# Performance work log

Hardware: AMD Instinct MI355X
Metric: run time of the kernel (lower is better)

Reference implementation:

```python
import jax, jax.numpy as jnp
import numpy as np
import math

B, S, D, H = 2, 2048, 1024, 16
DH = D // H

def setup_inputs() -> dict:
    key = jax.random.key(0)
    ks = jax.random.split(key, 16)
    g = lambda k, shp, s=1.0: jax.random.normal(k, shp, dtype=jnp.float32) * s
    w = 1.0 / math.sqrt(D)
    return {
        "x": g(ks[0], (B, S, D)),
        "pos_emb": g(ks[1], (S, D)),
        "Wq": g(ks[2], (D, D), w), "bq": g(ks[3], (D,), 0.02),
        "Wk": g(ks[4], (D, D), w), "bk": g(ks[5], (D,), 0.02),
        "Wv": g(ks[6], (D, D), w), "bv": g(ks[7], (D,), 0.02),
        "Wo": g(ks[8], (D, D), w), "bo": g(ks[9], (D,), 0.02),
        "Wkr": g(ks[10], (D, D), w), "bkr": g(ks[11], (D,), 0.02),
        "u": g(ks[12], (H, DH)),
        "v": g(ks[13], (H, DH)),
    }

def _relative_shift(t):
    # t: [b, h, s, L] -> pad one zero column at front, reinterpret as
    # [b, h, L+1, s], drop first row -> [b, h, L, s] (matches torch view_as trick)
    b, h, s, L = t.shape
    t = jnp.pad(t, ((0, 0), (0, 0), (0, 0), (1, 0)))
    t = t.reshape(b, h, L + 1, s)
    return t[:, :, 1:, :]

def reference(x, pos_emb, Wq, bq, Wk, bk, Wv, bv, Wo, bo, Wkr, bkr, u, v):
    b, s, d = x.shape
    scale = 1.0 / math.sqrt(DH)
    # projections (memory=None, so keys/values come from x itself)
    q = (x @ Wq + bq).reshape(b, s, H, DH).transpose(0, 2, 1, 3)   # [b,h,s,dh]
    k = (x @ Wk + bk).reshape(b, s, H, DH).transpose(0, 2, 1, 3)   # [b,h,s,dh]
    val = (x @ Wv + bv).reshape(b, s, H, DH).transpose(0, 2, 1, 3)  # [b,h,s,dh]
    k_r = (pos_emb @ Wkr + bkr).reshape(s, H, DH)                   # [L,h,dh]
    # four score terms
    AC = jnp.einsum('bhid,bhjd->bhij', q, k)                         # [b,h,s,L]
    BD = _relative_shift(jnp.einsum('bhid,jhd->bhij', q, k_r))       # [b,h,L,s] (s==L)
    EF = jnp.einsum('hd,bhjd->bhj', u, k)[:, :, None, :]             # [b,h,1,L]
    GH = _relative_shift(jnp.einsum('hd,jhd->hj', v, k_r)[None, :, None, :])  # [1,h,L,1]
    attn_score = (AC + BD + EF + GH) * scale
    attn_prob = jax.nn.softmax(attn_score, axis=-1)
    out = jnp.einsum('bhij,bhjd->bhid', attn_prob, val)              # [b,h,s,dh]
    out = out.transpose(0, 2, 1, 3).reshape(b, s, d)
    return out @ Wo + bo
```

## Files before the change

kernel.cpp:

```cpp
#include <hip/hip_runtime.h>
#include <hip/hip_bf16.h>

#define S_LEN 2048
#define D_MODEL 1024
#define NH 16
#define DHEAD 64
#define NB 2

typedef __attribute__((ext_vector_type(8))) short bf16x8;
typedef __attribute__((ext_vector_type(4))) float f32x4;

__device__ __forceinline__ float bf2f(unsigned short u) {
    return __uint_as_float(((unsigned)u) << 16);
}
__device__ __forceinline__ unsigned short f2bf(float f) {
    unsigned x = __float_as_uint(f);
    x += 0x7fffu + ((x >> 16) & 1u);
    return (unsigned short)(x >> 16);
}

__global__ __launch_bounds__(256)
void convert_bf16(const float* __restrict__ in, unsigned short* __restrict__ out, int n4) {
    int i = blockIdx.x * 256 + threadIdx.x;
    if (i >= n4) return;
    float4 v = reinterpret_cast<const float4*>(in)[i];
    ushort4 o;
    o.x = f2bf(v.x); o.y = f2bf(v.y); o.z = f2bf(v.z); o.w = f2bf(v.w);
    reinterpret_cast<ushort4*>(out)[i] = o;
}

__global__ __launch_bounds__(256)
void convert_transpose(const float* __restrict__ in, unsigned short* __restrict__ out) {
    __shared__ float t[32][33];
    int k0 = blockIdx.y * 32, n0 = blockIdx.x * 32;
    int tx = threadIdx.x & 31, ty = threadIdx.x >> 5;
    #pragma unroll
    for (int r = ty; r < 32; r += 8) t[r][tx] = in[(size_t)(k0 + r) * D_MODEL + n0 + tx];
    __syncthreads();
    #pragma unroll
    for (int r = ty; r < 32; r += 8) out[(size_t)(n0 + r) * D_MODEL + k0 + tx] = f2bf(t[tx][r]);
}

template<int MODE>
__global__ __launch_bounds__(256)
void gemm_mfma(const unsigned short* __restrict__ A,
               const unsigned short* __restrict__ Wt,
               const float* __restrict__ bias,
               void* __restrict__ C, int M) {
    const int K = D_MODEL;
    __shared__ short As[128][72];
    __shared__ short Bs[128][72];
    int tid = threadIdx.x;
    int m0 = blockIdx.y * 128, n0 = blockIdx.x * 128;
    int lane = tid & 63, w = tid >> 6;
    int wm = (w >> 1) * 64, wn = (w & 1) * 64;
    int ls = lane & 15, lg = lane >> 4;

    f32x4 acc[4][4];
    #pragma unroll
    for (int ms = 0; ms < 4; ++ms)
        #pragma unroll
        for (int ns = 0; ns < 4; ++ns)
            acc[ms][ns] = (f32x4){0.f, 0.f, 0.f, 0.f};

    for (int k0 = 0; k0 < K; k0 += 64) {
        #pragma unroll
        for (int it = 0; it < 4; ++it) {
            int id = tid + it * 256;
            int row = id >> 3, ch = (id & 7) * 8;
            *reinterpret_cast<bf16x8*>(&As[row][ch]) =
                *reinterpret_cast<const bf16x8*>(A + (size_t)(m0 + row) * K + k0 + ch);
            *reinterpret_cast<bf16x8*>(&Bs[row][ch]) =
                *reinterpret_cast<const bf16x8*>(Wt + (size_t)(n0 + row) * K + k0 + ch);
        }
        __syncthreads();
        #pragma unroll
        for (int kk = 0; kk < 64; kk += 32) {
            bf16x8 af[4], bf[4];
            #pragma unroll
            for (int s = 0; s < 4; ++s) {
                af[s] = *reinterpret_cast<const bf16x8*>(&As[wm + s * 16 + ls][kk + lg * 8]);
                bf[s] = *reinterpret_cast<const bf16x8*>(&Bs[wn + s * 16 + ls][kk + lg * 8]);
            }
            #pragma unroll
            for (int ms = 0; ms < 4; ++ms)
                #pragma unroll
                for (int ns = 0; ns < 4; ++ns)
                    acc[ms][ns] = __builtin_amdgcn_mfma_f32_16x16x32_bf16(af[ms], bf[ns], acc[ms][ns], 0, 0, 0);
        }
        __syncthreads();
    }

    #pragma unroll
    for (int ns = 0; ns < 4; ++ns) {
        int n = n0 + wn + ns * 16 + ls;
        float bv = bias[n];
        #pragma unroll
        for (int ms = 0; ms < 4; ++ms) {
            #pragma unroll
            for (int e = 0; e < 4; ++e) {
                int m = m0 + wm + ms * 16 + lg * 4 + e;
                float v = acc[ms][ns][e] + bv;
                if (MODE == 0) {
                    ((float*)C)[(size_t)m * D_MODEL + n] = v;
                } else if (MODE == 1) {
                    int b = m >> 11, s = m & 2047, hh = n >> 6, dd = n & 63;
                    ((unsigned short*)C)[(((size_t)(b * NH + hh)) * S_LEN + s) * DHEAD + dd] = f2bf(v);
                } else if (MODE == 2) {
                    int s = m, hh = n >> 6, dd = n & 63;
                    ((unsigned short*)C)[(((size_t)hh) * S_LEN + s) * DHEAD + dd] = f2bf(v);
                } else {
                    int b = m >> 11, s = m & 2047, hh = n >> 6, dd = n & 63;
                    ((unsigned short*)C)[(((size_t)(b * NH + hh)) * DHEAD + dd) * S_LEN + s] = f2bf(v);
                }
            }
        }
    }
}

__global__ __launch_bounds__(256)
void ef_gh_kernel(const float* __restrict__ uv,
                  const unsigned short* __restrict__ kmat,
                  float* __restrict__ out, int total) {
    int idx = blockIdx.x * 256 + threadIdx.x;
    if (idx >= total) return;
    int pos = idx & (S_LEN - 1);
    int grp = idx >> 11;
    int hh = grp & (NH - 1);
    const unsigned short* krow = kmat + ((size_t)grp * S_LEN + pos) * DHEAD;
    const float* urow = uv + hh * DHEAD;
    float s = 0.f;
    #pragma unroll
    for (int d4 = 0; d4 < DHEAD; d4 += 4) {
        ushort4 kk = *reinterpret_cast<const ushort4*>(krow + d4);
        float4 uu = *reinterpret_cast<const float4*>(urow + d4);
        s += bf2f(kk.x) * uu.x + bf2f(kk.y) * uu.y
           + bf2f(kk.z) * uu.z + bf2f(kk.w) * uu.w;
    }
    out[idx] = s;
}

__global__ __launch_bounds__(256, 3)
void flash_mfma(const unsigned short* __restrict__ qT,
                const unsigned short* __restrict__ kT,
                const unsigned short* __restrict__ vTt,
                const unsigned short* __restrict__ krT,
                const float* __restrict__ EF,
                const float* __restrict__ GH,
                unsigned short* __restrict__ attn) {
    __shared__ unsigned short Ks[64][72];
    __shared__ unsigned short Vt[64][72];
    __shared__ unsigned short KRXU[128][72];
    __shared__ unsigned short Dp[65][68];
    __shared__ unsigned short Qs64[72];
    __shared__ float ef_s[64];
    __shared__ float gh_s[64];

    unsigned short* Pb = &KRXU[0][0];

    int tid = threadIdx.x;
    int bid = blockIdx.x;
    int ib = bid & 31;
    int bh = bid >> 5;
    int h = bh & (NH - 1);
    int b = bh >> 4;
    int i0 = ib * 64;

    int lane = tid & 63;
    int w = tid >> 6;
    int ls = lane & 15, lg = lane >> 4;

    const unsigned short* qbase = qT + (size_t)bh * S_LEN * DHEAD;
    const unsigned short* kbase = kT + (size_t)bh * S_LEN * DHEAD;
    const unsigned short* vtbase = vTt + (size_t)bh * DHEAD * S_LEN;
    const unsigned short* krbase = krT + (size_t)h * S_LEN * DHEAD;
    const float* efrow = EF + (size_t)bh * S_LEN;
    const float* ghrow = GH + (size_t)h * S_LEN;

    if (tid < 64) gh_s[tid] = ghrow[i0 + tid];
    if (tid < 8) {
        bf16x8 val = (bf16x8){0, 0, 0, 0, 0, 0, 0, 0};
        if (i0 + 64 < S_LEN)
            val = *reinterpret_cast<const bf16x8*>(qbase + (size_t)(i0 + 64) * DHEAD + tid * 8);
        *reinterpret_cast<bf16x8*>(&Qs64[tid * 8]) = val;
    }

    bf16x8 aq[2];
    #pragma unroll
    for (int kki = 0; kki < 2; ++kki)
        aq[kki] = *reinterpret_cast<const bf16x8*>(qbase + (size_t)(i0 + 16 * w + ls) * DHEAD + kki * 32 + lg * 8);

    f32x4 acc_o[4];
    #pragma unroll
    for (int nt = 0; nt < 4; ++nt) acc_o[nt] = (f32x4){0.f, 0.f, 0.f, 0.f};
    float m_r[4], l_r[4];
    #pragma unroll
    for (int e = 0; e < 4; ++e) { m_r[e] = -1e30f; l_r[e] = 0.f; }

    int nt0 = 3 - w;

    for (int jt = 0; jt < S_LEN / 64; ++jt) {
        int j0 = jt * 64;
        int dj = j0 - i0;

        #pragma unroll
        for (int it = 0; it < 2; ++it) {
            int s2 = tid + it * 256;
            int r = s2 >> 3, c8 = (s2 & 7) * 8;
            *reinterpret_cast<bf16x8*>(&Ks[r][c8]) =
                *reinterpret_cast<const bf16x8*>(kbase + (size_t)(j0 + r) * DHEAD + c8);
            *reinterpret_cast<bf16x8*>(&Vt[r][c8]) =
                *reinterpret_cast<const bf16x8*>(vtbase + (size_t)r * S_LEN + j0 + c8);
        }
        #pragma unroll
        for (int it = 0; it < 4; ++it) {
            int s2 = tid + it * 256;
            int v = s2 >> 3, c8 = (s2 & 7) * 8;
            int t = v + dj - 64;
            int gk = (t <= 0) ? (S_LEN - 1 + t) : (t - 1);
            bf16x8 val = (bf16x8){0, 0, 0, 0, 0, 0, 0, 0};
            if (gk >= 0)
                val = *reinterpret_cast<const bf16x8*>(krbase + (size_t)gk * DHEAD + c8);
            *reinterpret_cast<bf16x8*>(&KRXU[v][c8]) = val;
        }
        if (tid < 64) ef_s[tid] = efrow[j0 + tid];
        __syncthreads();

        f32x4 acc_ac[4];
        f32x4 acc_bd[5];
        #pragma unroll
        for (int nt = 0; nt < 4; ++nt) acc_ac[nt] = (f32x4){0.f, 0.f, 0.f, 0.f};
        #pragma unroll
        for (int i = 0; i < 5; ++i) acc_bd[i] = (f32x4){0.f, 0.f, 0.f, 0.f};

        #pragma unroll
        for (int kki = 0; kki < 2; ++kki) {
            #pragma unroll
            for (int nt = 0; nt < 4; ++nt) {
                bf16x8 bk = *reinterpret_cast<const bf16x8*>(&Ks[nt * 16 + ls][kki * 32 + lg * 8]);
                acc_ac[nt] = __builtin_amdgcn_mfma_f32_16x16x32_bf16(aq[kki], bk, acc_ac[nt], 0, 0, 0);
            }
            #pragma unroll
            for (int i = 0; i < 5; ++i) {
                bf16x8 bx = *reinterpret_cast<const bf16x8*>(&KRXU[(nt0 + i) * 16 + ls][kki * 32 + lg * 8]);
                acc_bd[i] = __builtin_amdgcn_mfma_f32_16x16x32_bf16(aq[kki], bx, acc_bd[i], 0, 0, 0);
            }
        }
        #pragma unroll
        for (int i = 0; i < 5; ++i) {
            int v = (nt0 + i) * 16 + ls;
            #pragma unroll
            for (int e = 0; e < 4; ++e) {
                int r = 16 * w + lg * 4 + e;
                int c = v + r - 64;
                if ((unsigned)c < 64u) Dp[r][c] = f2bf(acc_bd[i][e]);
            }
        }
        if (w == 3) {
            float s = 0.f;
            #pragma unroll
            for (int k8 = 0; k8 < 8; ++k8) {
                bf16x8 q8 = *reinterpret_cast<const bf16x8*>(&Qs64[k8 * 8]);
                bf16x8 x8 = *reinterpret_cast<const bf16x8*>(&KRXU[lane][k8 * 8]);
                #pragma unroll
                for (int e = 0; e < 8; ++e)
                    s += bf2f((unsigned short)q8[e]) * bf2f((unsigned short)x8[e]);
            }
            Dp[64][lane] = f2bf(s);
        }
        __syncthreads();

        float pv[4][4];
        #pragma unroll
        for (int nt = 0; nt < 4; ++nt) {
            int jl = nt * 16 + ls;
            float efv = ef_s[jl];
            #pragma unroll
            for (int e = 0; e < 4; ++e) {
                int il = 16 * w + lg * 4 + e;
                int t = dj + jl - il;
                float bd = (t == 1) ? 0.f : (t <= 0 ? bf2f(Dp[il][jl]) : bf2f(Dp[il + 1][jl]));
                pv[nt][e] = (acc_ac[nt][e] + bd + efv + gh_s[il]) * 0.125f;
            }
        }
        float fr[4];
        #pragma unroll
        for (int e = 0; e < 4; ++e) {
            float tm = fmaxf(fmaxf(pv[0][e], pv[1][e]), fmaxf(pv[2][e], pv[3][e]));
            #pragma unroll
            for (int off = 8; off >= 1; off >>= 1) tm = fmaxf(tm, __shfl_xor(tm, off));
            float mnew = fmaxf(m_r[e], tm);
            float fe = __expf(m_r[e] - mnew);
            float rs = 0.f;
            #pragma unroll
            for (int nt = 0; nt < 4; ++nt) {
                pv[nt][e] = __expf(pv[nt][e] - mnew);
                rs += pv[nt][e];
            }
            #pragma unroll
            for (int off = 8; off >= 1; off >>= 1) rs += __shfl_xor(rs, off);
            l_r[e] = l_r[e] * fe + rs;
            m_r[e] = mnew;
            fr[e] = fe;
        }
        #pragma unroll
        for (int nt = 0; nt < 4; ++nt)
            #pragma unroll
            for (int e = 0; e < 4; ++e)
                Pb[(16 * w + lg * 4 + e) * 72 + nt * 16 + ls] = f2bf(pv[nt][e]);
        __syncthreads();

        #pragma unroll
        for (int nt = 0; nt < 4; ++nt)
            #pragma unroll
            for (int e = 0; e < 4; ++e)
                acc_o[nt][e] *= fr[e];
        #pragma unroll
        for (int kki = 0; kki < 2; ++kki) {
            bf16x8 ap = *reinterpret_cast<const bf16x8*>(&Pb[(16 * w + ls) * 72 + kki * 32 + lg * 8]);
            #pragma unroll
            for (int nt = 0; nt < 4; ++nt) {
                bf16x8 bv = *reinterpret_cast<const bf16x8*>(&Vt[nt * 16 + ls][kki * 32 + lg * 8]);
                acc_o[nt] = __builtin_amdgcn_mfma_f32_16x16x32_bf16(ap, bv, acc_o[nt], 0, 0, 0);
            }
        }
        __syncthreads();
    }

    #pragma unroll
    for (int nt = 0; nt < 4; ++nt) {
        int d = nt * 16 + ls;
        #pragma unroll
        for (int e = 0; e < 4; ++e) {
            int il = 16 * w + lg * 4 + e;
            float v = acc_o[nt][e] / l_r[e];
            attn[((size_t)b * S_LEN + i0 + il) * D_MODEL + h * DHEAD + d] = f2bf(v);
        }
    }
}

extern "C" void kernel_launch(void* const* d_in, const int* in_sizes, int n_in,
                              void* d_out, int out_size, void* d_ws, size_t ws_size,
                              hipStream_t stream) {
    const float* x    = (const float*)d_in[0];
    const float* pos  = (const float*)d_in[1];
    const float* Wq   = (const float*)d_in[2];
    const float* bq   = (const float*)d_in[3];
    const float* Wk   = (const float*)d_in[4];
    const float* bk   = (const float*)d_in[5];
    const float* Wv   = (const float*)d_in[6];
    const float* bv   = (const float*)d_in[7];
    const float* Wo   = (const float*)d_in[8];
    const float* bo   = (const float*)d_in[9];
    const float* Wkr  = (const float*)d_in[10];
    const float* bkr  = (const float*)d_in[11];
    const float* uu   = (const float*)d_in[12];
    const float* vv   = (const float*)d_in[13];

    char* w = (char*)d_ws;
    unsigned short* qT   = (unsigned short*)(w);
    unsigned short* kT   = (unsigned short*)(w + 8388608);
    unsigned short* vTt  = (unsigned short*)(w + 16777216);
    unsigned short* krT  = (unsigned short*)(w + 25165824);
    unsigned short* attn = (unsigned short*)(w + 29360128);
    float* EF            = (float*)(w + 37748736);
    float* GH            = (float*)(w + 38010880);
    unsigned short* xb   = (unsigned short*)(w + 38141952);
    unsigned short* posb = (unsigned short*)(w + 46530560);
    unsigned short* Wt   = (unsigned short*)(w + 50724864);

    dim3 blk(256);
    dim3 gT(32, 32);
    dim3 gBig(8, 32);
    dim3 gSm(8, 16);

    convert_bf16<<<4096, blk, 0, stream>>>(x, xb, 1048576);
    convert_bf16<<<2048, blk, 0, stream>>>(pos, posb, 524288);

    convert_transpose<<<gT, blk, 0, stream>>>(Wq, Wt);
    gemm_mfma<1><<<gBig, blk, 0, stream>>>(xb, Wt, bq, qT, 4096);
    convert_transpose<<<gT, blk, 0, stream>>>(Wk, Wt);
    gemm_mfma<1><<<gBig, blk, 0, stream>>>(xb, Wt, bk, kT, 4096);
    convert_transpose<<<gT, blk, 0, stream>>>(Wv, Wt);
    gemm_mfma<3><<<gBig, blk, 0, stream>>>(xb, Wt, bv, vTt, 4096);
    convert_transpose<<<gT, blk, 0, stream>>>(Wkr, Wt);
    gemm_mfma<2><<<gSm, blk, 0, stream>>>(posb, Wt, bkr, krT, 2048);

    ef_gh_kernel<<<(NB * NH * S_LEN) / 256, blk, 0, stream>>>(uu, kT, EF, NB * NH * S_LEN);
    ef_gh_kernel<<<(NH * S_LEN) / 256, blk, 0, stream>>>(vv, krT, GH, NH * S_LEN);

    flash_mfma<<<NB * NH * (S_LEN / 64), blk, 0, stream>>>(qT, kT, vTt, krT, EF, GH, attn);

    convert_transpose<<<gT, blk, 0, stream>>>(Wo, Wt);
    gemm_mfma<0><<<gBig, blk, 0, stream>>>(attn, Wt, bo, (float*)d_out, 4096);
}
```

Baseline: 585.3 us.

## Prefetch next K/V/Kr tiles into registers and use ring buffer for Kr

Restructures the flash attention loop to issue global loads for the next tile's K, V^T, relative-position keys and EF into registers before the current tile's compute, then store them to shared memory after the final barrier. The Kr shared buffer becomes a 128-row ring indexed by position modulo 128, so only 64 new rows are loaded per iteration instead of 128. The P staging buffer moves to the Ks region, and s_setprio wraps the MFMA sections. This hides global load latency behind compute at the cost of extra registers and a possible drop in occupancy.

```diff
diff --git a/kernel.cpp b/kernel.cpp
--- a/kernel.cpp
+++ b/kernel.cpp
@@ -156,7 +156,7 @@
     __shared__ float ef_s[64];
     __shared__ float gh_s[64];
 
-    unsigned short* Pb = &KRXU[0][0];
+    unsigned short* Pb = &Ks[0][0];
 
     int tid = threadIdx.x;
     int bid = blockIdx.x;
@@ -190,41 +190,64 @@
     for (int kki = 0; kki < 2; ++kki)
         aq[kki] = *reinterpret_cast<const bf16x8*>(qbase + (size_t)(i0 + 16 * w + ls) * DHEAD + kki * 32 + lg * 8);
 
-    f32x4 acc_o[4];
-    #pragma unroll
-    for (int nt = 0; nt < 4; ++nt) acc_o[nt] = (f32x4){0.f, 0.f, 0.f, 0.f};
-    float m_r[4], l_r[4];
-    #pragma unroll
-    for (int e = 0; e < 4; ++e) { m_r[e] = -1e30f; l_r[e] = 0.f; }
-
-    int nt0 = 3 - w;
-
-    for (int jt = 0; jt < S_LEN / 64; ++jt) {
-        int j0 = jt * 64;
-        int dj = j0 - i0;
-
+    {
+        int dj0 = -i0;
         #pragma unroll
         for (int it = 0; it < 2; ++it) {
             int s2 = tid + it * 256;
             int r = s2 >> 3, c8 = (s2 & 7) * 8;
             *reinterpret_cast<bf16x8*>(&Ks[r][c8]) =
-                *reinterpret_cast<const bf16x8*>(kbase + (size_t)(j0 + r) * DHEAD + c8);
+                *reinterpret_cast<const bf16x8*>(kbase + (size_t)r * DHEAD + c8);
             *reinterpret_cast<bf16x8*>(&Vt[r][c8]) =
-                *reinterpret_cast<const bf16x8*>(vtbase + (size_t)r * S_LEN + j0 + c8);
+                *reinterpret_cast<const bf16x8*>(vtbase + (size_t)r * S_LEN + c8);
         }
         #pragma unroll
         for (int it = 0; it < 4; ++it) {
             int s2 = tid + it * 256;
             int v = s2 >> 3, c8 = (s2 & 7) * 8;
-            int t = v + dj - 64;
+            int t = dj0 - 64 + v;
             int gk = (t <= 0) ? (S_LEN - 1 + t) : (t - 1);
             bf16x8 val = (bf16x8){0, 0, 0, 0, 0, 0, 0, 0};
             if (gk >= 0)
                 val = *reinterpret_cast<const bf16x8*>(krbase + (size_t)gk * DHEAD + c8);
-            *reinterpret_cast<bf16x8*>(&KRXU[v][c8]) = val;
-        }
-        if (tid < 64) ef_s[tid] = efrow[j0 + tid];
-        __syncthreads();
+            *reinterpret_cast<bf16x8*>(&KRXU[t & 127][c8]) = val;
+        }
+        if (tid < 64) ef_s[tid] = efrow[tid];
+    }
+
+    f32x4 acc_o[4];
+    #pragma unroll
+    for (int nt = 0; nt < 4; ++nt) acc_o[nt] = (f32x4){0.f, 0.f, 0.f, 0.f};
+    float m_r[4], l_r[4];
+    #pragma unroll
+    for (int e = 0; e < 4; ++e) { m_r[e] = -1e30f; l_r[e] = 0.f; }
+
+    int nt0 = 3 - w;
+    __syncthreads();
+
+    for (int jt = 0; jt < S_LEN / 64; ++jt) {
+        int j0 = jt * 64;
+        int dj = j0 - i0;
+        bool pf = (jt < S_LEN / 64 - 1);
+
+        bf16x8 kreg[2], vreg[2], xreg[2];
+        float efn = 0.f;
+        if (pf) {
+            int j0n = j0 + 64;
+            #pragma unroll
+            for (int it = 0; it < 2; ++it) {
+                int s2 = tid + it * 256;
+                int r = s2 >> 3, c8 = (s2 & 7) * 8;
+                kreg[it] = *reinterpret_cast<const bf16x8*>(kbase + (size_t)(j0n + r) * DHEAD + c8);
+                vreg[it] = *reinterpret_cast<const bf16x8*>(vtbase + (size_t)r * S_LEN + j0n + c8);
+                int t = dj + 64 + r;
+                int gk = (t <= 0) ? (S_LEN - 1 + t) : (t - 1);
+                xreg[it] = (bf16x8){0, 0, 0, 0, 0, 0, 0, 0};
+                if (gk >= 0)
+                    xreg[it] = *reinterpret_cast<const bf16x8*>(krbase + (size_t)gk * DHEAD + c8);
+            }
+            if (tid < 64) efn = efrow[j0n + tid];
+        }
 
         f32x4 acc_ac[4];
         f32x4 acc_bd[5];
@@ -233,6 +256,7 @@
         #pragma unroll
         for (int i = 0; i < 5; ++i) acc_bd[i] = (f32x4){0.f, 0.f, 0.f, 0.f};
 
+        __builtin_amdgcn_s_setprio(1);
         #pragma unroll
         for (int kki = 0; kki < 2; ++kki) {
             #pragma unroll
@@ -242,10 +266,12 @@
             }
             #pragma unroll
             for (int i = 0; i < 5; ++i) {
-                bf16x8 bx = *reinterpret_cast<const bf16x8*>(&KRXU[(nt0 + i) * 16 + ls][kki * 32 + lg * 8]);
+                int vrow = (dj - 64 + (nt0 + i) * 16) & 127;
+                bf16x8 bx = *reinterpret_cast<const bf16x8*>(&KRXU[vrow + ls][kki * 32 + lg * 8]);
                 acc_bd[i] = __builtin_amdgcn_mfma_f32_16x16x32_bf16(aq[kki], bx, acc_bd[i], 0, 0, 0);
             }
         }
+        __builtin_amdgcn_s_setprio(0);
         #pragma unroll
         for (int i = 0; i < 5; ++i) {
             int v = (nt0 + i) * 16 + ls;
@@ -258,10 +284,11 @@
         }
         if (w == 3) {
             float s = 0.f;
+            int prow = (dj - 64 + lane) & 127;
             #pragma unroll
             for (int k8 = 0; k8 < 8; ++k8) {
                 bf16x8 q8 = *reinterpret_cast<const bf16x8*>(&Qs64[k8 * 8]);
-                bf16x8 x8 = *reinterpret_cast<const bf16x8*>(&KRXU[lane][k8 * 8]);
+                bf16x8 x8 = *reinterpret_cast<const bf16x8*>(&KRXU[prow][k8 * 8]);
                 #pragma unroll
                 for (int e = 0; e < 8; ++e)
                     s += bf2f((unsigned short)q8[e]) * bf2f((unsigned short)x8[e]);
@@ -315,6 +342,7 @@
             #pragma unroll
             for (int e = 0; e < 4; ++e)
                 acc_o[nt][e] *= fr[e];
+        __builtin_amdgcn_s_setprio(1);
         #pragma unroll
         for (int kki = 0; kki < 2; ++kki) {
             bf16x8 ap = *reinterpret_cast<const bf16x8*>(&Pb[(16 * w + ls) * 72 + kki * 32 + lg * 8]);
@@ -324,7 +352,22 @@
                 acc_o[nt] = __builtin_amdgcn_mfma_f32_16x16x32_bf16(ap, bv, acc_o[nt], 0, 0, 0);
             }
         }
+        __builtin_amdgcn_s_setprio(0);
         __syncthreads();
+
+        if (pf) {
+            #pragma unroll
+            for (int it = 0; it < 2; ++it) {
+                int s2 = tid + it * 256;
+                int r = s2 >> 3, c8 = (s2 & 7) * 8;
+                *reinterpret_cast<bf16x8*>(&Ks[r][c8]) = kreg[it];
+                *reinterpret_cast<bf16x8*>(&Vt[r][c8]) = vreg[it];
+                int t = dj + 64 + r;
+                *reinterpret_cast<bf16x8*>(&KRXU[t & 127][c8]) = xreg[it];
+            }
+            if (tid < 64) ef_s[tid] = efn;
+            __syncthreads();
+        }
     }
 
     #pragma unroll
```

Result: no change. 596.3 us (+1.9%).
